# Performance work log

Hardware: AMD Instinct MI355X
Metric: run time of the kernel (lower is better)

## Reference

```python
import jax, jax.numpy as jnp
import numpy as np

D = 1024
H = 16
HD = D // H
FF = 4096
EPS = 1e-5


def setup_inputs() -> dict:
    key = jax.random.key(0)
    ks = jax.random.split(key, 12)
    s = lambda fan_in: 1.0 / np.sqrt(fan_in)
    return {
        "x": jax.random.normal(ks[0], (8, 1024, D), dtype=jnp.float32),
        "ln1_g": jnp.ones((D,), jnp.float32),
        "ln1_b": jnp.zeros((D,), jnp.float32),
        "ln2_g": jnp.ones((D,), jnp.float32),
        "ln2_b": jnp.zeros((D,), jnp.float32),
        "qkv_w": jax.random.uniform(ks[1], (3 * D, D), jnp.float32, -s(D), s(D)),
        "q_bias": jnp.zeros((D,), jnp.float32),
        "v_bias": jnp.zeros((D,), jnp.float32),
        "proj_w": jax.random.uniform(ks[2], (D, D), jnp.float32, -s(D), s(D)),
        "proj_b": jnp.zeros((D,), jnp.float32),
        "fc1_w": jax.random.uniform(ks[3], (FF, D), jnp.float32, -s(D), s(D)),
        "fc1_b": jnp.zeros((FF,), jnp.float32),
        "fc2_w": jax.random.uniform(ks[4], (D, FF), jnp.float32, -s(FF), s(FF)),
        "fc2_b": jnp.zeros((D,), jnp.float32),
    }


def _layernorm(x, g, b):
    mu = jnp.mean(x, axis=-1, keepdims=True)
    var = jnp.mean(jnp.square(x - mu), axis=-1, keepdims=True)
    return (x - mu) * jax.lax.rsqrt(var + EPS) * g + b


def reference(x, ln1_g, ln1_b, ln2_g, ln2_b, qkv_w, q_bias, v_bias,
              proj_w, proj_b, fc1_w, fc1_b, fc2_w, fc2_b):
    b, n, d = x.shape
    scale = HD ** (-0.5)
    # --- attention branch ---
    h = _layernorm(x, ln1_g, ln1_b)
    qkv_bias = jnp.concatenate([q_bias, jnp.zeros_like(v_bias), v_bias])
    qkv = h @ qkv_w.T + qkv_bias  # [b, n, 3d]
    qkv = qkv.reshape(b, n, 3, H, HD).transpose(2, 0, 3, 1, 4)  # [3, b, h, n, hd]
    q, k, v = qkv[0], qkv[1], qkv[2]
    attn = jnp.einsum("bhnd,bhmd->bhnm", q * scale, k)
    attn = jax.nn.softmax(attn, axis=-1)
    o = jnp.einsum("bhnm,bhmd->bhnd", attn, v)
    o = o.transpose(0, 2, 1, 3).reshape(b, n, d)
    x = x + (o @ proj_w.T + proj_b)
    # --- mlp branch ---
    h = _layernorm(x, ln2_g, ln2_b)
    h = jax.nn.gelu(h @ fc1_w.T + fc1_b, approximate=False)
    x = x + (h @ fc2_w.T + fc2_b)
    return x
```

## Files before the change

### kernel.cpp

```cpp
#include <hip/hip_runtime.h>
#include <hip/hip_bf16.h>


typedef __attribute__((ext_vector_type(8))) short short8;
typedef __attribute__((ext_vector_type(4))) float floatx4;

__device__ __forceinline__ unsigned short f2bf(float f) {
  union { __hip_bfloat16 h; unsigned short u; } cv;
  cv.h = __float2bfloat16(f);
  return cv.u;
}

__device__ __forceinline__ float fast_exp2(float x) {
  return __builtin_amdgcn_exp2f(x);
}

__device__ __forceinline__ void async_ld16(const void* g, void* l) {
  __builtin_amdgcn_global_load_lds(
      (const __attribute__((address_space(1))) unsigned int*)g,
      (__attribute__((address_space(3))) unsigned int*)l, 16, 0, 0);
}

__global__ __launch_bounds__(256) void cvt_bf16(const float* __restrict__ in,
                                                unsigned short* __restrict__ out) {
  const long i = ((long)blockIdx.x * 256 + threadIdx.x) * 4;
  const float4 v = *(const float4*)(in + i);
  ushort4 o;
  o.x = f2bf(v.x); o.y = f2bf(v.y); o.z = f2bf(v.z); o.w = f2bf(v.w);
  *(ushort4*)(out + i) = o;
}

__global__ __launch_bounds__(256) void ln_bf16(const float* __restrict__ x,
                                               const float* __restrict__ g,
                                               const float* __restrict__ b,
                                               unsigned short* __restrict__ out) {
  const int row = blockIdx.x;
  const int tid = threadIdx.x;
  const float4 v = ((const float4*)(x + (long)row * 1024))[tid];
  float s = v.x + v.y + v.z + v.w;
  float ss = v.x * v.x + v.y * v.y + v.z * v.z + v.w * v.w;
#pragma unroll
  for (int off = 1; off < 64; off <<= 1) {
    s += __shfl_xor(s, off);
    ss += __shfl_xor(ss, off);
  }
  __shared__ float red[8];
  const int wave = tid >> 6, lane = tid & 63;
  if (lane == 0) { red[wave] = s; red[4 + wave] = ss; }
  __syncthreads();
  if (tid == 0) {
    red[0] = red[0] + red[1] + red[2] + red[3];
    red[4] = red[4] + red[5] + red[6] + red[7];
  }
  __syncthreads();
  const float mu = red[0] * (1.f / 1024.f);
  const float var = red[4] * (1.f / 1024.f) - mu * mu;
  const float rstd = rsqrtf(var + 1e-5f);
  const int c = tid * 4;
  ushort4 o;
  o.x = f2bf((v.x - mu) * rstd * g[c + 0] + b[c + 0]);
  o.y = f2bf((v.y - mu) * rstd * g[c + 1] + b[c + 1]);
  o.z = f2bf((v.z - mu) * rstd * g[c + 2] + b[c + 2]);
  o.w = f2bf((v.w - mu) * rstd * g[c + 3] + b[c + 3]);
  ((ushort4*)(out + (long)row * 1024))[tid] = o;
}

#define BM 128
#define BN 128

template <int MODE>
__global__ __launch_bounds__(256) void gemm_bt(
    const unsigned short* __restrict__ A, const unsigned short* __restrict__ B,
    int M, int N, int Kd,
    const float* __restrict__ b0, const float* __restrict__ b1,
    const float* __restrict__ resid,
    void* __restrict__ out0, void* __restrict__ out1, void* __restrict__ out2) {
  __shared__ unsigned short lA[2][2][BM * 32];
  __shared__ unsigned short lB[2][2][BN * 32];
  const int tid = threadIdx.x;
  const int wave = tid >> 6, lane = tid & 63;
  const int l16 = lane & 15, quad = lane >> 4;
  const int wr = wave >> 1, wc = wave & 1;
  const int bid = blockIdx.x;
  const int xcd = bid & 7;
  const int s = bid >> 3;
  const long m0 = (long)(xcd * 8 + (s & 7)) * BM;
  const long n0 = (long)(s >> 3) * BN;

  const int row = tid >> 2;
  const int kc = (tid & 3) ^ ((row >> 1) & 3);
  const unsigned short* aSrc = A + (m0 + row) * Kd + kc * 8;
  const unsigned short* bSrc = B + (n0 + row) * Kd + kc * 8;
  const int ldsOff0 = wave * 1024;
  const int ldsOff1 = wave * 1024 + 4096;

  floatx4 acc[4][4];
#pragma unroll
  for (int i = 0; i < 4; i++)
#pragma unroll
    for (int j = 0; j < 4; j++) acc[i][j] = (floatx4){0.f, 0.f, 0.f, 0.f};

#pragma unroll
  for (int sb = 0; sb < 2; sb++) {
    async_ld16(aSrc + sb * 32, (char*)&lA[0][sb][0] + ldsOff0);
    async_ld16(aSrc + 64 * Kd + sb * 32, (char*)&lA[0][sb][0] + ldsOff1);
    async_ld16(bSrc + sb * 32, (char*)&lB[0][sb][0] + ldsOff0);
    async_ld16(bSrc + 64 * Kd + sb * 32, (char*)&lB[0][sb][0] + ldsOff1);
  }

  const int sw = ((l16 >> 1) & 3);

  for (int k0 = 0; k0 < Kd; k0 += 64) {
    const int buf = (k0 >> 6) & 1;
    __syncthreads();
    const int kn = k0 + 64;
    if (kn < Kd) {
#pragma unroll
      for (int sb = 0; sb < 2; sb++) {
        async_ld16(aSrc + kn + sb * 32, (char*)&lA[buf ^ 1][sb][0] + ldsOff0);
        async_ld16(aSrc + 64 * Kd + kn + sb * 32,
                   (char*)&lA[buf ^ 1][sb][0] + ldsOff1);
        async_ld16(bSrc + kn + sb * 32, (char*)&lB[buf ^ 1][sb][0] + ldsOff0);
        async_ld16(bSrc + 64 * Kd + kn + sb * 32,
                   (char*)&lB[buf ^ 1][sb][0] + ldsOff1);
      }
    }
#pragma unroll
    for (int sb = 0; sb < 2; sb++) {
      short8 af[4], bfv[4];
#pragma unroll
      for (int mi = 0; mi < 4; mi++) {
        const int r = wr * 64 + mi * 16 + l16;
        af[mi] = *(const short8*)(&lA[buf][sb][(r * 4 + (quad ^ sw)) * 8]);
      }
#pragma unroll
      for (int ni = 0; ni < 4; ni++) {
        const int r = wc * 64 + ni * 16 + l16;
        bfv[ni] = *(const short8*)(&lB[buf][sb][(r * 4 + (quad ^ sw)) * 8]);
      }
#pragma unroll
      for (int mi = 0; mi < 4; mi++)
#pragma unroll
        for (int ni = 0; ni < 4; ni++)
          acc[mi][ni] = __builtin_amdgcn_mfma_f32_16x16x32_bf16(
              af[mi], bfv[ni], acc[mi][ni], 0, 0, 0);
    }
  }

#pragma unroll
  for (int mi = 0; mi < 4; mi++) {
    const long rbase = m0 + wr * 64 + mi * 16 + quad * 4;
#pragma unroll
    for (int ni = 0; ni < 4; ni++) {
      const long cg = n0 + wc * 64 + ni * 16 + l16;
#pragma unroll
      for (int reg = 0; reg < 4; reg++) {
        const long rr = rbase + reg;
        const float val = acc[mi][ni][reg];
        if (MODE == 0) {
          const int which = (int)(cg >> 10);
          const int col = (int)(cg & 1023);
          const int bidx = (int)(rr >> 10), t = (int)(rr & 1023);
          const int head = col >> 6, hd = col & 63;
          const long bh = bidx * 16 + head;
          if (which == 0) {
            ((unsigned short*)out0)[(bh * 1024 + t) * 64 + hd] =
                f2bf((val + b0[col]) * 0.1803368801111244f);
          } else if (which == 1) {
            ((unsigned short*)out1)[(bh * 1024 + t) * 64 + hd] = f2bf(val);
          } else {
            ((unsigned short*)out2)[(bh * 64 + hd) * 1024 + t] =
                f2bf(val + b1[col]);
          }
        } else if (MODE == 1) {
          const long idx = rr * N + cg;
          ((float*)out0)[idx] = resid[idx] + val + b0[cg];
        } else {
          const float u = val + b0[cg];
          const float gl = 0.5f * u * (1.0f + erff(u * 0.70710678118f));
          ((unsigned short*)out0)[rr * N + cg] = f2bf(gl);
        }
      }
    }
  }
}

__global__ __launch_bounds__(256) void attn(const unsigned short* __restrict__ Q,
                                            const unsigned short* __restrict__ Kc,
                                            const unsigned short* __restrict__ Vt,
                                            unsigned short* __restrict__ O) {
  __shared__ unsigned short lK[2][2048];
  __shared__ unsigned short lV[2][2048];
  __shared__ float P[4][2][16][34];
  const int tid = threadIdx.x;
  const int wave = tid >> 6, lane = tid & 63;
  const int l16 = lane & 15, quad = lane >> 4;
  const int bid = blockIdx.x;
  const int xcd = bid & 7;
  const int sl = bid >> 3;
  const int bh = xcd * 16 + (sl & 15);
  const int q0 = (sl >> 4) * 128 + wave * 32;
  const unsigned short* Qb = Q + ((long)bh * 1024 + q0) * 64;
  const unsigned short* Kb = Kc + (long)bh * 65536;
  const unsigned short* Vb = Vt + (long)bh * 65536;

  short8 qf[2][2];
#pragma unroll
  for (int t = 0; t < 2; t++)
#pragma unroll
    for (int h = 0; h < 2; h++)
      qf[t][h] = *(const short8*)(Qb + (t * 16 + l16) * 64 + h * 32 + quad * 8);

  const int kr = tid >> 3;
  const int kc = (tid & 7) ^ (kr & 7);
  const unsigned short* kSrc = Kb + kr * 64 + kc * 8;
  const int vr = tid >> 2;
  const int vc = (tid & 3) ^ (vr & 3) ^ ((vr >> 2) & 3);
  const unsigned short* vSrc = Vb + vr * 1024 + vc * 8;

  floatx4 oacc[2][4];
#pragma unroll
  for (int t = 0; t < 2; t++)
#pragma unroll
    for (int u = 0; u < 4; u++) oacc[t][u] = (floatx4){0.f, 0.f, 0.f, 0.f};
  float lrun[2][4] = {{0.f, 0.f, 0.f, 0.f}, {0.f, 0.f, 0.f, 0.f}};

  async_ld16(kSrc, (char*)&lK[0][0] + wave * 1024);
  async_ld16(vSrc, (char*)&lV[0][0] + wave * 1024);

  const int vca = quad ^ (l16 & 3) ^ ((l16 >> 2) & 3);

  for (int ks = 0; ks < 1024; ks += 32) {
    const int buf = (ks >> 5) & 1;
    __syncthreads();
    const int kn = ks + 32;
    if (kn < 1024) {
      async_ld16(kSrc + kn * 64, (char*)&lK[buf ^ 1][0] + wave * 1024);
      async_ld16(vSrc + kn,      (char*)&lV[buf ^ 1][0] + wave * 1024);
    }
    short8 kf[2][2];
#pragma unroll
    for (int i = 0; i < 2; i++)
#pragma unroll
      for (int h = 0; h < 2; h++) {
        const int gr = (i * 16 + l16) * 8 + ((h * 4 + quad) ^ (l16 & 7));
        kf[i][h] = *(const short8*)(&lK[buf][gr * 8]);
      }
    floatx4 s[2][2];
#pragma unroll
    for (int t = 0; t < 2; t++)
#pragma unroll
      for (int i = 0; i < 2; i++) {
        const floatx4 z = {0.f, 0.f, 0.f, 0.f};
        floatx4 a = __builtin_amdgcn_mfma_f32_16x16x32_bf16(qf[t][0], kf[i][0], z, 0, 0, 0);
        s[t][i] = __builtin_amdgcn_mfma_f32_16x16x32_bf16(qf[t][1], kf[i][1], a, 0, 0, 0);
      }
#pragma unroll
    for (int t = 0; t < 2; t++)
#pragma unroll
      for (int r = 0; r < 4; r++) {
        const float p0 = fast_exp2(s[t][0][r]);
        const float p1 = fast_exp2(s[t][1][r]);
        lrun[t][r] += p0 + p1;
        P[wave][t][quad * 4 + r][l16] = p0;
        P[wave][t][quad * 4 + r][16 + l16] = p1;
      }
    short8 vf[4];
#pragma unroll
    for (int u = 0; u < 4; u++)
      vf[u] = *(const short8*)(&lV[buf][((u * 16 + l16) * 4 + vca) * 8]);
    short8 pf[2];
#pragma unroll
    for (int t = 0; t < 2; t++) {
      const float* pr = &P[wave][t][l16][quad * 8];
      const floatx4 pa = *(const floatx4*)pr;
      const floatx4 pb = *(const floatx4*)(pr + 4);
      pf[t][0] = (short)f2bf(pa[0]); pf[t][1] = (short)f2bf(pa[1]);
      pf[t][2] = (short)f2bf(pa[2]); pf[t][3] = (short)f2bf(pa[3]);
      pf[t][4] = (short)f2bf(pb[0]); pf[t][5] = (short)f2bf(pb[1]);
      pf[t][6] = (short)f2bf(pb[2]); pf[t][7] = (short)f2bf(pb[3]);
    }
#pragma unroll
    for (int t = 0; t < 2; t++)
#pragma unroll
      for (int u = 0; u < 4; u++)
        oacc[t][u] = __builtin_amdgcn_mfma_f32_16x16x32_bf16(pf[t], vf[u], oacc[t][u], 0, 0, 0);
  }

  const int b = bh >> 4, h = bh & 15;
#pragma unroll
  for (int t = 0; t < 2; t++) {
#pragma unroll
    for (int r = 0; r < 4; r++) {
      float lr = lrun[t][r];
      lr += __shfl_xor(lr, 1);
      lr += __shfl_xor(lr, 2);
      lr += __shfl_xor(lr, 4);
      lr += __shfl_xor(lr, 8);
      const float linv = 1.0f / lr;
#pragma unroll
      for (int u = 0; u < 4; u++) {
        O[((long)b * 1024 + q0 + t * 16 + quad * 4 + r) * 1024 + h * 64 + u * 16 + l16] =
            f2bf(oacc[t][u][r] * linv);
      }
    }
  }
}

extern "C" void kernel_launch(void* const* d_in, const int* in_sizes, int n_in,
                              void* d_out, int out_size, void* d_ws, size_t ws_size,
                              hipStream_t stream) {
  const float* x      = (const float*)d_in[0];
  const float* ln1_g  = (const float*)d_in[1];
  const float* ln1_b  = (const float*)d_in[2];
  const float* ln2_g  = (const float*)d_in[3];
  const float* ln2_b  = (const float*)d_in[4];
  const float* qkv_w  = (const float*)d_in[5];
  const float* q_bias = (const float*)d_in[6];
  const float* v_bias = (const float*)d_in[7];
  const float* proj_w = (const float*)d_in[8];
  const float* proj_b = (const float*)d_in[9];
  const float* fc1_w  = (const float*)d_in[10];
  const float* fc1_b  = (const float*)d_in[11];
  const float* fc2_w  = (const float*)d_in[12];
  const float* fc2_b  = (const float*)d_in[13];
  float* out = (float*)d_out;

  char* ws = (char*)d_ws;
  unsigned short* Wqkv  = (unsigned short*)(ws);
  unsigned short* Wproj = (unsigned short*)(ws + 6291456);
  unsigned short* Wfc1  = (unsigned short*)(ws + 8388608);
  unsigned short* Wfc2  = (unsigned short*)(ws + 16777216);
  float*          X1    = (float*)        (ws + 25165824);
  unsigned short* Hbuf  = (unsigned short*)(ws + 58720256);
  unsigned short* Qbuf  = (unsigned short*)(ws + 75497472);
  unsigned short* Kbuf  = (unsigned short*)(ws + 92274688);
  unsigned short* Vtbuf = (unsigned short*)(ws + 109051904);
  unsigned short* Obuf  = (unsigned short*)(ws + 125829120);
  unsigned short* ACT   = Qbuf;

  cvt_bf16<<<3072 * 1024 / 1024, 256, 0, stream>>>(qkv_w, Wqkv);
  cvt_bf16<<<1024 * 1024 / 1024, 256, 0, stream>>>(proj_w, Wproj);
  cvt_bf16<<<4096 * 1024 / 1024, 256, 0, stream>>>(fc1_w, Wfc1);
  cvt_bf16<<<4096 * 1024 / 1024, 256, 0, stream>>>(fc2_w, Wfc2);

  ln_bf16<<<8192, 256, 0, stream>>>(x, ln1_g, ln1_b, Hbuf);
  gemm_bt<0><<<24 * 64, 256, 0, stream>>>(Hbuf, Wqkv, 8192, 3072, 1024,
                                          q_bias, v_bias, nullptr,
                                          Qbuf, Kbuf, Vtbuf);
  attn<<<1024, 256, 0, stream>>>(Qbuf, Kbuf, Vtbuf, Obuf);
  gemm_bt<1><<<8 * 64, 256, 0, stream>>>(Obuf, Wproj, 8192, 1024, 1024,
                                         proj_b, nullptr, x,
                                         X1, nullptr, nullptr);
  ln_bf16<<<8192, 256, 0, stream>>>(X1, ln2_g, ln2_b, Hbuf);
  gemm_bt<2><<<32 * 64, 256, 0, stream>>>(Hbuf, Wfc1, 8192, 4096, 1024,
                                          fc1_b, nullptr, nullptr,
                                          ACT, nullptr, nullptr);
  gemm_bt<1><<<8 * 64, 256, 0, stream>>>(ACT, Wfc2, 8192, 1024, 4096,
                                         fc2_b, nullptr, X1,
                                         out, nullptr, nullptr);
  (void)in_sizes; (void)n_in; (void)out_size; (void)ws_size;
}
```

Baseline: 565.9 us.

## Add 256x256-tile 8-wave GEMM with staged LDS pipeline for QKV and FC1

Adds a new GEMM kernel that uses 256x256 output tiles, 512 threads and a K-step of 64, with split half-tile async LDS staging interleaved between MFMA quadrants. Barriers and s_setprio are used to overlap global-to-LDS loads with compute. It is used for the QKV and FC1 projections, which have large N. The aim is more data reuse per loaded byte and better hiding of load latency. The cost is higher register pressure, fewer blocks for tile-level parallelism, and a more fragile hand-written wait/barrier schedule.

Measured after the change: 586.1 us. 1.04x slower.

```diff
diff --git a/kernel.cpp b/kernel.cpp
--- a/kernel.cpp
+++ b/kernel.cpp
@@ -20,6 +20,8 @@
       (const __attribute__((address_space(1))) unsigned int*)g,
       (__attribute__((address_space(3))) unsigned int*)l, 16, 0, 0);
 }
+
+#define VMCNT(n) asm volatile("s_waitcnt vmcnt(" #n ")" ::: "memory")
 
 __global__ __launch_bounds__(256) void cvt_bf16(const float* __restrict__ in,
                                                 unsigned short* __restrict__ out) {
@@ -63,6 +65,36 @@
   o.z = f2bf((v.z - mu) * rstd * g[c + 2] + b[c + 2]);
   o.w = f2bf((v.w - mu) * rstd * g[c + 3] + b[c + 3]);
   ((ushort4*)(out + (long)row * 1024))[tid] = o;
+}
+
+template <int MODE>
+__device__ __forceinline__ void epi_store(
+    long rr, long cg, float val, int N,
+    const float* __restrict__ b0, const float* __restrict__ b1,
+    const float* __restrict__ resid,
+    void* __restrict__ out0, void* __restrict__ out1, void* __restrict__ out2) {
+  if (MODE == 0) {
+    const int which = (int)(cg >> 10);
+    const int col = (int)(cg & 1023);
+    const int bidx = (int)(rr >> 10), t = (int)(rr & 1023);
+    const int head = col >> 6, hd = col & 63;
+    const long bh = bidx * 16 + head;
+    if (which == 0) {
+      ((unsigned short*)out0)[(bh * 1024 + t) * 64 + hd] =
+          f2bf((val + b0[col]) * 0.1803368801111244f);
+    } else if (which == 1) {
+      ((unsigned short*)out1)[(bh * 1024 + t) * 64 + hd] = f2bf(val);
+    } else {
+      ((unsigned short*)out2)[(bh * 64 + hd) * 1024 + t] = f2bf(val + b1[col]);
+    }
+  } else if (MODE == 1) {
+    const long idx = rr * N + cg;
+    ((float*)out0)[idx] = resid[idx] + val + b0[cg];
+  } else {
+    const float u = val + b0[cg];
+    const float gl = 0.5f * u * (1.0f + erff(u * 0.70710678118f));
+    ((unsigned short*)out0)[rr * N + cg] = f2bf(gl);
+  }
 }
 
 #define BM 128
@@ -154,35 +186,142 @@
     for (int ni = 0; ni < 4; ni++) {
       const long cg = n0 + wc * 64 + ni * 16 + l16;
 #pragma unroll
-      for (int reg = 0; reg < 4; reg++) {
-        const long rr = rbase + reg;
-        const float val = acc[mi][ni][reg];
-        if (MODE == 0) {
-          const int which = (int)(cg >> 10);
-          const int col = (int)(cg & 1023);
-          const int bidx = (int)(rr >> 10), t = (int)(rr & 1023);
-          const int head = col >> 6, hd = col & 63;
-          const long bh = bidx * 16 + head;
-          if (which == 0) {
-            ((unsigned short*)out0)[(bh * 1024 + t) * 64 + hd] =
-                f2bf((val + b0[col]) * 0.1803368801111244f);
-          } else if (which == 1) {
-            ((unsigned short*)out1)[(bh * 1024 + t) * 64 + hd] = f2bf(val);
-          } else {
-            ((unsigned short*)out2)[(bh * 64 + hd) * 1024 + t] =
-                f2bf(val + b1[col]);
-          }
-        } else if (MODE == 1) {
-          const long idx = rr * N + cg;
-          ((float*)out0)[idx] = resid[idx] + val + b0[cg];
-        } else {
-          const float u = val + b0[cg];
-          const float gl = 0.5f * u * (1.0f + erff(u * 0.70710678118f));
-          ((unsigned short*)out0)[rr * N + cg] = f2bf(gl);
-        }
-      }
-    }
-  }
+      for (int reg = 0; reg < 4; reg++)
+        epi_store<MODE>(rbase + reg, cg, acc[mi][ni][reg], N, b0, b1, resid,
+                        out0, out1, out2);
+    }
+  }
+  (void)M;
+}
+
+template <int MODE>
+__global__ __launch_bounds__(512, 2) void gemm256(
+    const unsigned short* __restrict__ A, const unsigned short* __restrict__ B,
+    int M, int N, int Kd,
+    const float* __restrict__ b0, const float* __restrict__ b1,
+    const float* __restrict__ resid,
+    void* __restrict__ out0, void* __restrict__ out1, void* __restrict__ out2) {
+  __shared__ __align__(16) unsigned short lds[2][4][2][4096];
+  const int tid = threadIdx.x;
+  const int wave = tid >> 6, lane = tid & 63;
+  const int l16 = lane & 15, quad = lane >> 4;
+  const int wr = wave >> 2, wc = wave & 3;
+  const int bid = blockIdx.x;
+  const int xcd = bid & 7, s = bid >> 3;
+  const long m0 = (long)(xcd * 4 + (s & 3)) * 256;
+  const long n0 = (long)(s >> 2) * 256;
+  const int NT = Kd >> 6;
+
+  const int srow = tid >> 2;
+  const int skc = (tid & 3) ^ ((srow >> 1) & 3);
+  const unsigned short* aS = A + (m0 + srow) * Kd + skc * 8;
+  const unsigned short* bS = B + (n0 + srow) * Kd + skc * 8;
+  const unsigned short* aS1 = aS + 128 * (long)Kd;
+  const unsigned short* bS1 = bS + 128 * (long)Kd;
+  const int wvOff = wave * 1024;
+
+#define STG(half, src, t, bp)                                                \
+  do {                                                                       \
+    async_ld16((src) + ((long)(t) << 6),                                     \
+               (char*)&lds[bp][half][0][0] + wvOff);                         \
+    async_ld16((src) + ((long)(t) << 6) + 32,                                \
+               (char*)&lds[bp][half][1][0] + wvOff);                         \
+  } while (0)
+
+  floatx4 acc[8][4];
+#pragma unroll
+  for (int i = 0; i < 8; i++)
+#pragma unroll
+    for (int j = 0; j < 4; j++) acc[i][j] = (floatx4){0.f, 0.f, 0.f, 0.f};
+
+  short8 af[4][2];
+  short8 bf[4][2];
+  const int sw = (l16 >> 1) & 3;
+
+#define RDA(qm)                                                              \
+  _Pragma("unroll") for (int mi = 0; mi < 4; mi++) {                         \
+    const int r = (qm)*64 + mi * 16 + l16;                                   \
+    _Pragma("unroll") for (int kk = 0; kk < 2; kk++)                         \
+        af[mi][kk] = *(const short8*)(                                       \
+            &lds[buf][wr][kk][(r * 4 + (quad ^ sw)) * 8]);                   \
+  }
+#define RDB(pair)                                                            \
+  _Pragma("unroll") for (int j = 0; j < 2; j++) {                            \
+    const int ni = (pair)*2 + j;                                             \
+    const int r = (wc & 1) * 64 + ni * 16 + l16;                             \
+    _Pragma("unroll") for (int kk = 0; kk < 2; kk++)                         \
+        bf[ni][kk] = *(const short8*)(                                       \
+            &lds[buf][2 + (wc >> 1)][kk][(r * 4 + (quad ^ sw)) * 8]);        \
+  }
+#define MFMA_Q(qm, qn)                                                       \
+  __builtin_amdgcn_s_setprio(1);                                             \
+  _Pragma("unroll") for (int mi = 0; mi < 4; mi++) {                         \
+    _Pragma("unroll") for (int j = 0; j < 2; j++) {                          \
+      floatx4 c_ = acc[(qm)*4 + mi][(qn)*2 + j];                             \
+      c_ = __builtin_amdgcn_mfma_f32_16x16x32_bf16(af[mi][0],                \
+                                                   bf[(qn)*2 + j][0], c_,    \
+                                                   0, 0, 0);                 \
+      c_ = __builtin_amdgcn_mfma_f32_16x16x32_bf16(af[mi][1],                \
+                                                   bf[(qn)*2 + j][1], c_,    \
+                                                   0, 0, 0);                 \
+      acc[(qm)*4 + mi][(qn)*2 + j] = c_;                                     \
+    }                                                                        \
+  }                                                                          \
+  __builtin_amdgcn_s_setprio(0);
+#define LGKM0                                                                \
+  asm volatile("s_waitcnt lgkmcnt(0)" ::: "memory");                         \
+  __builtin_amdgcn_sched_barrier(0);
+
+  STG(0, aS, 0, 0); STG(1, aS1, 0, 0); STG(2, bS, 0, 0); STG(3, bS1, 0, 0);
+  STG(2, bS, 1, 1); STG(3, bS1, 1, 1); STG(0, aS, 1, 1);
+  VMCNT(6);
+  __builtin_amdgcn_s_barrier();
+
+  for (int t = 0; t < NT; ++t) {
+    const int buf = t & 1, nxt = buf ^ 1;
+    RDA(0);
+    RDB(0);
+    if (t + 1 < NT) STG(1, aS1, t + 1, nxt);
+    __builtin_amdgcn_s_barrier();
+    LGKM0;
+    MFMA_Q(0, 0);
+    __builtin_amdgcn_s_barrier();
+    RDB(1);
+    __builtin_amdgcn_s_barrier();
+    LGKM0;
+    MFMA_Q(0, 1);
+    __builtin_amdgcn_s_barrier();
+    RDA(1);
+    if (t + 2 < NT) STG(2, bS, t + 2, buf);
+    __builtin_amdgcn_s_barrier();
+    LGKM0;
+    MFMA_Q(1, 1);
+    __builtin_amdgcn_s_barrier();
+    if (t + 2 < NT) { STG(3, bS1, t + 2, buf); STG(0, aS, t + 2, buf); }
+    __builtin_amdgcn_s_barrier();
+    MFMA_Q(1, 0);
+    if (t + 2 < NT) { VMCNT(6); } else { VMCNT(0); }
+    __builtin_amdgcn_s_barrier();
+  }
+
+#pragma unroll
+  for (int mi2 = 0; mi2 < 8; mi2++) {
+    const long rbase = m0 + wr * 128 + mi2 * 16 + quad * 4;
+#pragma unroll
+    for (int nj = 0; nj < 4; nj++) {
+      const long cg = n0 + wc * 64 + nj * 16 + l16;
+#pragma unroll
+      for (int reg = 0; reg < 4; reg++)
+        epi_store<MODE>(rbase + reg, cg, acc[mi2][nj][reg], N, b0, b1, resid,
+                        out0, out1, out2);
+    }
+  }
+  (void)M;
+#undef STG
+#undef RDA
+#undef RDB
+#undef MFMA_Q
+#undef LGKM0
 }
 
 __global__ __launch_bounds__(256) void attn(const unsigned short* __restrict__ Q,
@@ -246,21 +385,21 @@
         const int gr = (i * 16 + l16) * 8 + ((h * 4 + quad) ^ (l16 & 7));
         kf[i][h] = *(const short8*)(&lK[buf][gr * 8]);
       }
-    floatx4 s[2][2];
+    floatx4 sres[2][2];
 #pragma unroll
     for (int t = 0; t < 2; t++)
 #pragma unroll
       for (int i = 0; i < 2; i++) {
         const floatx4 z = {0.f, 0.f, 0.f, 0.f};
         floatx4 a = __builtin_amdgcn_mfma_f32_16x16x32_bf16(qf[t][0], kf[i][0], z, 0, 0, 0);
-        s[t][i] = __builtin_amdgcn_mfma_f32_16x16x32_bf16(qf[t][1], kf[i][1], a, 0, 0, 0);
+        sres[t][i] = __builtin_amdgcn_mfma_f32_16x16x32_bf16(qf[t][1], kf[i][1], a, 0, 0, 0);
       }
 #pragma unroll
     for (int t = 0; t < 2; t++)
 #pragma unroll
       for (int r = 0; r < 4; r++) {
-        const float p0 = fast_exp2(s[t][0][r]);
-        const float p1 = fast_exp2(s[t][1][r]);
+        const float p0 = fast_exp2(sres[t][0][r]);
+        const float p1 = fast_exp2(sres[t][1][r]);
         lrun[t][r] += p0 + p1;
         P[wave][t][quad * 4 + r][l16] = p0;
         P[wave][t][quad * 4 + r][16 + l16] = p1;
@@ -345,17 +484,17 @@
   cvt_bf16<<<4096 * 1024 / 1024, 256, 0, stream>>>(fc2_w, Wfc2);
 
   ln_bf16<<<8192, 256, 0, stream>>>(x, ln1_g, ln1_b, Hbuf);
-  gemm_bt<0><<<24 * 64, 256, 0, stream>>>(Hbuf, Wqkv, 8192, 3072, 1024,
-                                          q_bias, v_bias, nullptr,
-                                          Qbuf, Kbuf, Vtbuf);
+  gemm256<0><<<384, 512, 0, stream>>>(Hbuf, Wqkv, 8192, 3072, 1024,
+                                      q_bias, v_bias, nullptr,
+                                      Qbuf, Kbuf, Vtbuf);
   attn<<<1024, 256, 0, stream>>>(Qbuf, Kbuf, Vtbuf, Obuf);
   gemm_bt<1><<<8 * 64, 256, 0, stream>>>(Obuf, Wproj, 8192, 1024, 1024,
                                          proj_b, nullptr, x,
                                          X1, nullptr, nullptr);
   ln_bf16<<<8192, 256, 0, stream>>>(X1, ln2_g, ln2_b, Hbuf);
-  gemm_bt<2><<<32 * 64, 256, 0, stream>>>(Hbuf, Wfc1, 8192, 4096, 1024,
-                                          fc1_b, nullptr, nullptr,
-                                          ACT, nullptr, nullptr);
+  gemm256<2><<<512, 512, 0, stream>>>(Hbuf, Wfc1, 8192, 4096, 1024,
+                                      fc1_b, nullptr, nullptr,
+                                      ACT, nullptr, nullptr);
   gemm_bt<1><<<8 * 64, 256, 0, stream>>>(ACT, Wfc2, 8192, 1024, 4096,
                                          fc2_b, nullptr, X1,
                                          out, nullptr, nullptr);
```
